# Optimization experiments

Hardware: AMD Instinct MI355X
Metric: run time of the kernel (lower is better)

## Reference

```python
import jax, jax.numpy as jnp
import numpy as np

N, E, H, HEADS, L, B = 16000, 256000, 192, 4, 4, 8
C = H // HEADS
VN, VE, T = 32, 8, 1000


def _sin_emb(t, dim):
    half = dim // 2
    freqs = jnp.exp(-np.log(10000.0) * jnp.arange(half, dtype=jnp.float32) / half)
    ang = t.astype(jnp.float32)[:, None] * freqs[None, :]
    return jnp.concatenate([jnp.sin(ang), jnp.cos(ang)], axis=-1)


def _ln(x, g, b, eps=1e-5):
    mu = jnp.mean(x, -1, keepdims=True)
    var = jnp.mean(jnp.square(x - mu), -1, keepdims=True)
    return (x - mu) * jax.lax.rsqrt(var + eps) * g + b


def setup_inputs():
    key = jax.random.key(0)
    ks = iter(jax.random.split(key, 64))
    p = lambda shape, s=0.02: jax.random.normal(next(ks), shape, jnp.float32) * s
    inp = {}
    inp['node_emb'] = p((VN, H))
    inp['edge_emb'] = p((VE, H))
    inp['time_w1'] = p((H, H)); inp['time_b1'] = jnp.zeros((H,), jnp.float32)
    inp['time_w2'] = p((H, H)); inp['time_b2'] = jnp.zeros((H,), jnp.float32)
    inp['mask_emb'] = p((2, H))
    inp['wq'] = p((L, H, H)); inp['bq'] = jnp.zeros((L, H), jnp.float32)
    inp['wk'] = p((L, H, H)); inp['bk'] = jnp.zeros((L, H), jnp.float32)
    inp['wv'] = p((L, H, H)); inp['bv'] = jnp.zeros((L, H), jnp.float32)
    inp['we'] = p((L, H, H))
    inp['wskip'] = p((L, H, H)); inp['bskip'] = jnp.zeros((L, H), jnp.float32)
    inp['wbeta'] = p((L, 3 * H))
    inp['ln_g'] = jnp.ones((L, H), jnp.float32); inp['ln_b'] = jnp.zeros((L, H), jnp.float32)
    inp['node_out_w'] = p((H, VN)); inp['node_out_b'] = jnp.zeros((VN,), jnp.float32)
    inp['edge_w1'] = p((4 * H, H)); inp['edge_b1'] = jnp.zeros((H,), jnp.float32)
    inp['edge_w2'] = p((H, VE)); inp['edge_b2'] = jnp.zeros((VE,), jnp.float32)
    inp['node_type'] = jax.random.randint(next(ks), (N,), 0, VN)
    inp['edge_type'] = jax.random.randint(next(ks), (E,), 0, VE)
    inp['edge_index'] = jax.random.randint(next(ks), (2, E), 0, N)
    inp['edit_mask'] = jax.random.randint(next(ks), (N,), 0, 2, dtype=jnp.int32)
    inp['node_batch'] = jnp.sort(jax.random.randint(next(ks), (N,), 0, B))
    inp['t_graph'] = jax.random.randint(next(ks), (B,), 1, T)
    return inp


def reference(node_emb, edge_emb, time_w1, time_b1, time_w2, time_b2, mask_emb,
              wq, bq, wk, bk, wv, bv, we, wskip, bskip, wbeta, ln_g, ln_b,
              node_out_w, node_out_b, edge_w1, edge_b1, edge_w2, edge_b2,
              node_type, edge_type, edge_index, edit_mask, node_batch, t_graph):
    src, dst = edge_index[0], edge_index[1]
    # time embedding: sinusoidal -> Linear -> SiLU -> Linear  => [B, H]
    t_vec = jax.nn.silu(_sin_emb(t_graph, H) @ time_w1 + time_b1) @ time_w2 + time_b2
    t_node = t_vec[node_batch]              # [N, H]
    t_edge = t_vec[node_batch[src]]         # [E, H]
    x = node_emb[node_type] + t_node + mask_emb[edit_mask]
    edge_attr = edge_emb[edge_type] + t_edge
    scale = 1.0 / np.sqrt(C)
    for l in range(L):
        q = (x @ wq[l] + bq[l]).reshape(N, HEADS, C)
        k = (x @ wk[l] + bk[l]).reshape(N, HEADS, C)
        v = (x @ wv[l] + bv[l]).reshape(N, HEADS, C)
        e = (edge_attr @ we[l]).reshape(E, HEADS, C)
        kj = k[src] + e                                   # [E, heads, C]
        score = jnp.sum(q[dst] * kj, axis=-1) * scale      # [E, heads]
        m = jax.ops.segment_max(score, dst, num_segments=N)
        ex = jnp.exp(score - m[dst])
        denom = jax.ops.segment_sum(ex, dst, num_segments=N)
        alpha = ex / denom[dst]
        msg = (v[src] + e) * alpha[..., None]              # [E, heads, C]
        out = jax.ops.segment_sum(msg, dst, num_segments=N).reshape(N, H)
        xr = x @ wskip[l] + bskip[l]
        beta = jax.nn.sigmoid(jnp.concatenate([out, xr, out - xr], -1) @ wbeta[l])[:, None]
        h = beta * xr + (1.0 - beta) * out
        x = _ln(x + h, ln_g[l], ln_b[l])
    node_logits = x @ node_out_w + node_out_b
    edge_feat = jnp.concatenate([x[src], x[dst], edge_attr, t_edge], -1)  # [E, 4H]
    edge_logits = jax.nn.silu(edge_feat @ edge_w1 + edge_b1) @ edge_w2 + edge_b2
    return node_logits, edge_logits
```

## Files before the change

### kernel.cpp

```cpp
#include <hip/hip_runtime.h>
#include <hip/hip_bf16.h>
#include <math.h>

#define NN 16000
#define NPAD 16128
#define NE 256000
#define H 192
#define RP 256
#define KVR 512
#define NL 4
#define NBATCH 8
#define VEt 8
#define HH (H*H)
#define EML 16

typedef __hip_bfloat16 bf16;
typedef unsigned short u16;
typedef unsigned char u8;
typedef unsigned int u32;
typedef __attribute__((ext_vector_type(8))) short bfrag_t;
typedef __attribute__((ext_vector_type(4))) float facc_t;
typedef __attribute__((ext_vector_type(4))) float f4;
typedef __attribute__((ext_vector_type(2))) unsigned int u32x2;

__device__ __forceinline__ bf16 f2b(float v){ return __float2bfloat16(v); }
__device__ __forceinline__ int rfl(int v){ return __builtin_amdgcn_readfirstlane(v); }

__device__ __forceinline__ unsigned enc8sw(float x){
    unsigned u = __float_as_uint(x);
    unsigned s = (u >> 24) & 0x80u;
    float ax = fabsf(x);
    if(ax >= 448.f) return s | 0x7Eu;
    if(ax < 0.015625f){
        int q = (int)rintf(ax * 512.f);
        return s | (unsigned)q;
    }
    unsigned au = u & 0x7FFFFFFFu;
    unsigned lsb = (au >> 20) & 1u;
    au += 0x7FFFFu + lsb;
    unsigned E = (au >> 23) - 127u;
    unsigned M = (au >> 20) & 7u;
    if((int)E > 8) return s | 0x7Eu;
    return s | ((E + 7u) << 3) | M;
}
__device__ __forceinline__ unsigned enc8(float x){
#if __has_builtin(__builtin_amdgcn_cvt_pk_fp8_f32)
    return (u32)__builtin_amdgcn_cvt_pk_fp8_f32(x, x, 0, false) & 0xFFu;
#else
    return enc8sw(x);
#endif
}
template<int SEL>
__device__ __forceinline__ float dec8s(u32 w){
#if __has_builtin(__builtin_amdgcn_cvt_f32_fp8)
    return __builtin_amdgcn_cvt_f32_fp8((int)w, SEL);
#else
    unsigned v = (w >> (SEL*8)) & 0xFFu;
    unsigned e = (v >> 3) & 15u, m = v & 7u;
    float mag = e ? __builtin_ldexpf((float)(8u + m), (int)e - 10)
                  : __builtin_ldexpf((float)m, -9);
    return (v & 0x80u) ? -mag : mag;
#endif
}
__device__ __forceinline__ float frcp(float x){
#if __has_builtin(__builtin_amdgcn_rcpf)
    return __builtin_amdgcn_rcpf(x);
#else
    return 1.f/x;
#endif
}

__global__ void k_sentinel(float* __restrict__ out, float v){ out[0] = v; }

__global__ void k_transpose(const float* __restrict__ wq, const float* __restrict__ wk,
                            const float* __restrict__ wv, const float* __restrict__ wsk,
                            const float* __restrict__ w1, const float* __restrict__ now,
                            const float* __restrict__ ew2, u16* __restrict__ wt){
    int mat = blockIdx.x;
    if(mat < 18){
        const float* src;
        if(mat < 4)       src = wq  + (size_t)mat*HH;
        else if(mat < 8)  src = wk  + (size_t)(mat-4)*HH;
        else if(mat < 12) src = wv  + (size_t)(mat-8)*HH;
        else if(mat < 16) src = wsk + (size_t)(mat-12)*HH;
        else              src = w1  + (size_t)(mat-16)*HH;
        u16* dst = wt + (size_t)mat*HH;
        const int slice = HH/8;
        int base = blockIdx.y*slice;
        for(int i = base + threadIdx.x; i < base + slice; i += blockDim.x){
            int k = i / H, n = i % H;
            bf16 b = f2b(src[i]);
            dst[n*H + k] = *(u16*)&b;
        }
    } else if(mat == 18){
        u16* dst = wt + (size_t)18*HH;
        const int slice = (32*192)/8;
        int base = blockIdx.y*slice;
        for(int i = base + threadIdx.x; i < base + slice; i += blockDim.x){
            int k = i >> 5, n = i & 31;
            bf16 b = f2b(now[i]);
            dst[n*192 + k] = *(u16*)&b;
        }
    } else {
        u16* dst = wt + (size_t)18*HH + 32*192;
        const int slice = (16*192)/8;
        int base = blockIdx.y*slice;
        for(int i = base + threadIdx.x; i < base + slice; i += blockDim.x){
            int k = i >> 4, n = i & 15;
            float v = (n < 8) ? ew2[k*8 + n] : 0.f;
            bf16 b = f2b(v);
            dst[n*192 + k] = *(u16*)&b;
        }
    }
}

__global__ void k_tvec(const int* __restrict__ tg, const float* __restrict__ w1,
                       const float* __restrict__ b1, const float* __restrict__ w2,
                       const float* __restrict__ b2, float* __restrict__ tvec){
    int b = blockIdx.x, j = threadIdx.x;
    __shared__ float emb[H], h1[H];
    float t = (float)tg[b];
    if(j < 96){
        float fr = __expf(-logf(10000.0f) * (float)j / 96.0f);
        float ang = t * fr;
        emb[j]      = sinf(ang);
        emb[j + 96] = cosf(ang);
    }
    __syncthreads();
    float acc = b1[j];
    for(int k = 0; k < H; k++) acc += emb[k] * w1[k*H + j];
    h1[j] = acc / (1.f + __expf(-acc));
    __syncthreads();
    float acc2 = b2[j];
    for(int k = 0; k < H; k++) acc2 += h1[k] * w2[k*H + j];
    tvec[b*H + j] = acc2;
}

__global__ void k_init_x(const float* __restrict__ nemb, const float* __restrict__ memb,
                         const float* __restrict__ tvec, const int* __restrict__ ntype,
                         const int* __restrict__ emask, const int* __restrict__ nbatch,
                         float* __restrict__ x, u16* __restrict__ xb){
    int idx = blockIdx.x*blockDim.x + threadIdx.x;
    if(idx >= NN*H) return;
    int n = idx / H, c = idx % H;
    float v = nemb[(size_t)ntype[n]*H + c] + tvec[nbatch[n]*H + c]
            + memb[(size_t)emask[n]*H + c];
    x[idx] = v;
    bf16 b = f2b(v); xb[idx] = *(u16*)&b;
}

__global__ void k_zero_i(int* __restrict__ p, int n){
    int i = blockIdx.x*blockDim.x + threadIdx.x;
    if(i < n) p[i] = 0;
}
__global__ void k_count(const int* __restrict__ edst, int* __restrict__ cnt){
    int e = blockIdx.x*blockDim.x + threadIdx.x;
    if(e < NE) atomicAdd(&cnt[edst[e]], 1);
}
__global__ __launch_bounds__(1024) void k_scan(const int* __restrict__ cnt,
                                               int* __restrict__ ofs, int* __restrict__ cur){
    __shared__ int wsum[16];
    __shared__ int carry_s;
    int tid = threadIdx.x, lane = tid & 63, w = tid >> 6;
    if(tid == 0) carry_s = 0;
    __syncthreads();
    for(int base = 0; base < NN; base += 1024){
        int idx = base + tid;
        int v = (idx < NN) ? cnt[idx] : 0;
        int sc = v;
        #pragma unroll
        for(int o = 1; o < 64; o <<= 1){
            int t = __shfl_up(sc, o);
            if(lane >= o) sc += t;
        }
        if(lane == 63) wsum[w] = sc;
        __syncthreads();
        if(w == 0){
            int ws = (lane < 16) ? wsum[lane] : 0;
            #pragma unroll
            for(int o = 1; o < 16; o <<= 1){
                int t = __shfl_up(ws, o);
                if(lane >= o) ws += t;
            }
            if(lane < 16) wsum[lane] = ws;
        }
        __syncthreads();
        int wbase = (w > 0) ? wsum[w-1] : 0;
        int c = carry_s;
        int excl = c + wbase + sc - v;
        if(idx < NN){ ofs[idx] = excl; cur[idx] = excl; }
        __syncthreads();
        if(tid == 0) carry_s = c + wsum[15];
        __syncthreads();
    }
    if(threadIdx.x == 0) ofs[NN] = carry_s;
}
__global__ void k_scatter(const int* __restrict__ esrc, const int* __restrict__ edst,
                          const int* __restrict__ etype, const int* __restrict__ nbatch,
                          int* __restrict__ cur, int2* __restrict__ spair){
    int e = blockIdx.x*blockDim.x + threadIdx.x;
    if(e >= NE) return;
    int s = esrc[e], d = edst[e];
    int pos = atomicAdd(&cur[d], 1);
    int2 se; se.x = s*KVR; se.y = (nbatch[s]*VEt + etype[e])*KVR;
    spair[pos] = se;
}

__global__ void k_etab(const float* __restrict__ eemb, const float* __restrict__ tvec,
                       const float* __restrict__ we, u16* __restrict__ etab){
    int blk = blockIdx.x;
    int l = blk >> 6, idx = blk & 63, b = idx >> 3, et = idx & 7;
    int c = threadIdx.x;
    __shared__ float a[H];
    a[c] = eemb[et*H + c] + tvec[b*H + c];
    __syncthreads();
    float acc = 0.f;
    const float* w = we + (size_t)l*HH;
    for(int k = 0; k < H; k++) acc += a[k] * w[k*H + c];
    bf16 bv = f2b(acc);
    etab[(size_t)blk*256 + (c/3)*4 + (c%3)] = *(u16*)&bv;
}

__global__ void k_ctab(const float* __restrict__ eemb, const float* __restrict__ tvec,
                       const float* __restrict__ w1, const float* __restrict__ b1,
                       u16* __restrict__ ctab){
    int idx = blockIdx.x, b = idx >> 3, et = idx & 7;
    int c = threadIdx.x;
    __shared__ float a[H];
    a[c] = eemb[et*H + c] + tvec[b*H + c];
    __syncthreads();
    float acc = b1[c];
    for(int k = 0; k < H; k++){
        acc += a[k]          * w1[(size_t)(2*H + k)*H + c];
        acc += tvec[b*H + k] * w1[(size_t)(3*H + k)*H + c];
    }
    bf16 bv = f2b(acc);
    ctab[(size_t)idx*256 + (c/3)*4 + (c%3)] = *(u16*)&bv;
}

struct GemmP {
    const u16* wt[4];
    const float* bias[4];
    void* out[4];
    int obf[4];
};
__global__ __launch_bounds__(256) void k_gemm(const u16* __restrict__ A, GemmP P){
    int oi = blockIdx.y / 3, nt = blockIdx.y % 3;
    const u16* Wt = P.wt[oi];
    const float* bias = P.bias[oi];
    int wave = rfl(threadIdx.x >> 6), lane = threadIdx.x & 63;
    int quad = lane >> 4, l16 = lane & 15;
    int m0 = blockIdx.x*256 + wave*64;
    int n0 = nt*64;
    facc_t acc[4][4];
    #pragma unroll
    for(int i = 0; i < 4; i++)
        #pragma unroll
        for(int j = 0; j < 4; j++){ acc[i][j][0]=0.f; acc[i][j][1]=0.f; acc[i][j][2]=0.f; acc[i][j][3]=0.f; }
    #pragma unroll
    for(int kc = 0; kc < 6; kc++){
        int kb = kc*32 + quad*8;
        bfrag_t af[4], bg[4];
        #pragma unroll
        for(int i = 0; i < 4; i++) af[i] = *(const bfrag_t*)(A  + (size_t)(m0 + i*16 + l16)*H + kb);
        #pragma unroll
        for(int j = 0; j < 4; j++) bg[j] = *(const bfrag_t*)(Wt + (size_t)(n0 + j*16 + l16)*H + kb);
        #pragma unroll
        for(int i = 0; i < 4; i++)
            #pragma unroll
            for(int j = 0; j < 4; j++)
                acc[i][j] = __builtin_amdgcn_mfma_f32_16x16x32_bf16(af[i], bg[j], acc[i][j], 0, 0, 0);
    }
    float bv[4];
    #pragma unroll
    for(int j = 0; j < 4; j++) bv[j] = bias ? bias[n0 + j*16 + l16] : 0.f;
    int mode = P.obf[oi];
    if(mode != 0){
        u8* out = (u8*)P.out[oi];
        int rstride = (mode == 2) ? RP : KVR;
        int mult    = (mode == 2) ? 4  : 8;
        int koff    = (mode == 4) ? 4  : 0;
        int byteoff[4];
        #pragma unroll
        for(int j = 0; j < 4; j++){
            int c = n0 + j*16 + l16;
            byteoff[j] = (c/3)*mult + (c%3) + koff;
        }
        #pragma unroll
        for(int i = 0; i < 4; i++){
            int rb = m0 + i*16 + quad*4;
            #pragma unroll
            for(int r = 0; r < 4; r++){
                int row = rb + r;
                if(row < NN){
                    #pragma unroll
                    for(int j = 0; j < 4; j++)
                        out[(size_t)row*rstride + byteoff[j]] = (u8)enc8(acc[i][j][r] + bv[j]);
                }
            }
        }
    } else {
        float* out = (float*)P.out[oi];
        #pragma unroll
        for(int i = 0; i < 4; i++){
            int rb = m0 + i*16 + quad*4;
            #pragma unroll
            for(int r = 0; r < 4; r++){
                int row = rb + r;
                if(row < NN){
                    #pragma unroll
                    for(int j = 0; j < 4; j++)
                        out[(size_t)row*H + n0 + j*16 + l16] = acc[i][j][r] + bv[j];
                }
            }
        }
    }
}

__global__ __launch_bounds__(256) void k_attn(
    const float* __restrict__ Q, const u8* __restrict__ KVb,
    const float* __restrict__ XR,
    const u16* __restrict__ etab, const int* __restrict__ ofs,
    const int2* __restrict__ spair,
    const float* __restrict__ wb, const float* __restrict__ lng, const float* __restrict__ lnb,
    float* __restrict__ x, u16* __restrict__ xb)
{
    int wv = rfl(threadIdx.x >> 6);
    int n = blockIdx.x*4 + wv;
    int lane = threadIdx.x & 63;
    int lane8 = lane*8;
    int ch = lane*3;
    size_t base = (size_t)n*H + ch;
    const float scale = 0.14433756729740646f;
    float q0 = Q[base], q1 = Q[base+1], q2 = Q[base+2];
    int p0 = ofs[n], p1 = ofs[n+1];
    float lac[4]  = {0.f,0.f,0.f,0.f};
    float ac0[4]  = {0.f,0.f,0.f,0.f};
    float ac1[4]  = {0.f,0.f,0.f,0.f};
    float ac2[4]  = {0.f,0.f,0.f,0.f};
    const u8* etb = (const u8*)etab;
    int p = p0;
    for(; p + 3 < p1; p += 4){
        int so[4], eo[4];
        #pragma unroll
        for(int t = 0; t < 4; t++){ so[t] = spair[p+t].x; eo[t] = spair[p+t].y; }
        u32x2 kv[4], ew[4];
        #pragma unroll
        for(int t = 0; t < 4; t++){
            kv[t] = *(const u32x2*)(KVb + so[t] + lane8);
            ew[t] = *(const u32x2*)(etb + eo[t] + lane8);
        }
        float e0[4], e1[4], e2[4], tt[4];
        #pragma unroll
        for(int t = 0; t < 4; t++){
            e0[t] = __uint_as_float(ew[t].x << 16);
            e1[t] = __uint_as_float(ew[t].x & 0xffff0000u);
            e2[t] = __uint_as_float(ew[t].y << 16);
            tt[t] = q0*(dec8s<0>(kv[t].x)+e0[t]) + q1*(dec8s<1>(kv[t].x)+e1[t])
                  + q2*(dec8s<2>(kv[t].x)+e2[t]);
        }
        #pragma unroll
        for(int o = 1; o <= 8; o <<= 1){
            #pragma unroll
            for(int t = 0; t < 4; t++) tt[t] += __shfl_xor(tt[t], o);
        }
        #pragma unroll
        for(int t = 0; t < 4; t++){
            float sc = fminf(fmaxf(tt[t]*scale, -60.f), 60.f);
            float pw = __expf(sc);
            lac[t] += pw;
            ac0[t] += pw*(dec8s<0>(kv[t].y)+e0[t]);
            ac1[t] += pw*(dec8s<1>(kv[t].y)+e1[t]);
            ac2[t] += pw*(dec8s<2>(kv[t].y)+e2[t]);
        }
    }
    for(; p < p1; p++){
        int soA = spair[p].x, eoA = spair[p].y;
        u32x2 kvA = *(const u32x2*)(KVb + soA + lane8);
        u32x2 ewA = *(const u32x2*)(etb + eoA + lane8);
        float e0A = __uint_as_float(ewA.x << 16);
        float e1A = __uint_as_float(ewA.x & 0xffff0000u);
        float e2A = __uint_as_float(ewA.y << 16);
        float tA = q0*(dec8s<0>(kvA.x)+e0A) + q1*(dec8s<1>(kvA.x)+e1A) + q2*(dec8s<2>(kvA.x)+e2A);
        tA += __shfl_xor(tA,1); tA += __shfl_xor(tA,2); tA += __shfl_xor(tA,4); tA += __shfl_xor(tA,8);
        float sc = fminf(fmaxf(tA*scale, -60.f), 60.f);
        float pw = __expf(sc);
        lac[0] += pw;
        ac0[0] += pw*(dec8s<0>(kvA.y)+e0A);
        ac1[0] += pw*(dec8s<1>(kvA.y)+e1A);
        ac2[0] += pw*(dec8s<2>(kvA.y)+e2A);
    }
    float l  = (lac[0]+lac[1]) + (lac[2]+lac[3]);
    float a0 = (ac0[0]+ac0[1]) + (ac0[2]+ac0[3]);
    float a1 = (ac1[0]+ac1[1]) + (ac1[2]+ac1[3]);
    float a2 = (ac2[0]+ac2[1]) + (ac2[2]+ac2[3]);
    float inv = (p1 > p0) ? 1.f/l : 0.f;
    float o0 = a0*inv, o1 = a1*inv, o2 = a2*inv;
    float xr0 = XR[base], xr1 = XR[base+1], xr2 = XR[base+2];
    float sd = o0*wb[ch]  + o1*wb[ch+1]  + o2*wb[ch+2]
             + xr0*wb[H+ch] + xr1*wb[H+ch+1] + xr2*wb[H+ch+2]
             + (o0-xr0)*wb[2*H+ch] + (o1-xr1)*wb[2*H+ch+1] + (o2-xr2)*wb[2*H+ch+2];
    sd += __shfl_xor(sd,1); sd += __shfl_xor(sd,2); sd += __shfl_xor(sd,4);
    sd += __shfl_xor(sd,8); sd += __shfl_xor(sd,16); sd += __shfl_xor(sd,32);
    float beta = 1.f/(1.f + __expf(-sd));
    float h0 = beta*xr0 + (1.f-beta)*o0;
    float h1 = beta*xr1 + (1.f-beta)*o1;
    float h2 = beta*xr2 + (1.f-beta)*o2;
    float y0 = x[base] + h0, y1 = x[base+1] + h1, y2 = x[base+2] + h2;
    float s3 = y0 + y1 + y2;
    float q3 = y0*y0 + y1*y1 + y2*y2;
    #pragma unroll
    for(int o = 1; o <= 32; o <<= 1){
        s3 += __shfl_xor(s3, o);
        q3 += __shfl_xor(q3, o);
    }
    float mean = s3 * (1.f/H);
    float var = fmaxf(q3*(1.f/H) - mean*mean, 0.f);
    float rs = rsqrtf(var + 1e-5f);
    float d0 = y0-mean, d1 = y1-mean, d2 = y2-mean;
    float z0 = d0*rs*lng[ch]   + lnb[ch];
    float z1 = d1*rs*lng[ch+1] + lnb[ch+1];
    float z2 = d2*rs*lng[ch+2] + lnb[ch+2];
    x[base] = z0; x[base+1] = z1; x[base+2] = z2;
    bf16 t0 = f2b(z0), t1 = f2b(z1), t2 = f2b(z2);
    xb[base] = *(u16*)&t0; xb[base+1] = *(u16*)&t1; xb[base+2] = *(u16*)&t2;
}

__global__ __launch_bounds__(256) void k_nodeout(const u16* __restrict__ A, const u16* __restrict__ Wt,
                                                 const float* __restrict__ b, float* __restrict__ out){
    int wave = rfl(threadIdx.x >> 6), lane = threadIdx.x & 63;
    int quad = lane >> 4, l16 = lane & 15;
    int m0 = blockIdx.x*256 + wave*64;
    facc_t acc[4][2];
    #pragma unroll
    for(int i = 0; i < 4; i++)
        #pragma unroll
        for(int j = 0; j < 2; j++){ acc[i][j][0]=0.f; acc[i][j][1]=0.f; acc[i][j][2]=0.f; acc[i][j][3]=0.f; }
    #pragma unroll
    for(int kc = 0; kc < 6; kc++){
        int kb = kc*32 + quad*8;
        bfrag_t af[4], bg[2];
        #pragma unroll
        for(int i = 0; i < 4; i++) af[i] = *(const bfrag_t*)(A  + (size_t)(m0 + i*16 + l16)*H + kb);
        #pragma unroll
        for(int j = 0; j < 2; j++) bg[j] = *(const bfrag_t*)(Wt + (size_t)(j*16 + l16)*H + kb);
        #pragma unroll
        for(int i = 0; i < 4; i++)
            #pragma unroll
            for(int j = 0; j < 2; j++)
                acc[i][j] = __builtin_amdgcn_mfma_f32_16x16x32_bf16(af[i], bg[j], acc[i][j], 0, 0, 0);
    }
    float bv[2];
    #pragma unroll
    for(int j = 0; j < 2; j++) bv[j] = b[j*16 + l16];
    #pragma unroll
    for(int i = 0; i < 4; i++){
        int rb = m0 + i*16 + quad*4;
        #pragma unroll
        for(int r = 0; r < 4; r++){
            int row = rb + r;
            if(row < NN){
                #pragma unroll
                for(int j = 0; j < 2; j++)
                    out[(size_t)row*32 + j*16 + l16] = acc[i][j][r] + bv[j];
            }
        }
    }
}

__global__ __launch_bounds__(256) void k_edgemlp(
    const int* __restrict__ esrc, const int* __restrict__ edst, const int* __restrict__ etype,
    const int* __restrict__ nb,
    const u8* __restrict__ xs1, const u8* __restrict__ xd1, const u16* __restrict__ ctab,
    const u16* __restrict__ w2t, const float* __restrict__ b2p, float* __restrict__ out)
{
    __shared__ u16 hbuf[4][16][200];
    int wave = rfl(threadIdx.x >> 6);
    int lane = threadIdx.x & 63;
    int lane8 = lane*8;
    int l16 = lane & 15, quad = lane >> 4;
    int wid = blockIdx.x*4 + wave;
    int e0 = wid*EML;
    const u8* ctb = (const u8*)ctab;
    bfrag_t bg[6];
    #pragma unroll
    for(int kc = 0; kc < 6; kc++)
        bg[kc] = *(const bfrag_t*)(w2t + (size_t)l16*192 + kc*32 + quad*8);
    for(int eb = 0; eb < EML; eb += 2){
        int eX = e0 + eb, eY = e0 + eb + 1;
        int sX = esrc[eX], dX = edst[eX];
        int sY = esrc[eY], dY = edst[eY];
        int coX = (nb[sX]*VEt + etype[eX])*KVR;
        int coY = (nb[sY]*VEt + etype[eY])*KVR;
        u32 awX = *(const u32*)(xs1 + (size_t)sX*RP + lane*4);
        u32 awY = *(const u32*)(xs1 + (size_t)sY*RP + lane*4);
        u32 bwX = *(const u32*)(xd1 + (size_t)dX*RP + lane*4);
        u32 bwY = *(const u32*)(xd1 + (size_t)dY*RP + lane*4);
        u32x2 cwX = *(const u32x2*)(ctb + coX + lane8);
        u32x2 cwY = *(const u32x2*)(ctb + coY + lane8);
        float cfX0 = __uint_as_float(cwX.x << 16);
        float cfX1 = __uint_as_float(cwX.x & 0xffff0000u);
        float cfX2 = __uint_as_float(cwX.y << 16);
        float cfY0 = __uint_as_float(cwY.x << 16);
        float cfY1 = __uint_as_float(cwY.x & 0xffff0000u);
        float cfY2 = __uint_as_float(cwY.y << 16);
        float hX0, hX1, hX2, hY0, hY1, hY2;
        { float v = dec8s<0>(awX)+dec8s<0>(bwX)+cfX0; hX0 = v*frcp(1.f+__expf(-v)); }
        { float v = dec8s<1>(awX)+dec8s<1>(bwX)+cfX1; hX1 = v*frcp(1.f+__expf(-v)); }
        { float v = dec8s<2>(awX)+dec8s<2>(bwX)+cfX2; hX2 = v*frcp(1.f+__expf(-v)); }
        { float v = dec8s<0>(awY)+dec8s<0>(bwY)+cfY0; hY0 = v*frcp(1.f+__expf(-v)); }
        { float v = dec8s<1>(awY)+dec8s<1>(bwY)+cfY1; hY1 = v*frcp(1.f+__expf(-v)); }
        { float v = dec8s<2>(awY)+dec8s<2>(bwY)+cfY2; hY2 = v*frcp(1.f+__expf(-v)); }
        u16* rowX = &hbuf[wave][eb][0];
        u16* rowY = &hbuf[wave][eb+1][0];
        bf16 x0 = f2b(hX0), x1 = f2b(hX1), x2 = f2b(hX2);
        bf16 y0 = f2b(hY0), y1 = f2b(hY1), y2 = f2b(hY2);
        rowX[lane*3+0] = *(u16*)&x0; rowX[lane*3+1] = *(u16*)&x1; rowX[lane*3+2] = *(u16*)&x2;
        rowY[lane*3+0] = *(u16*)&y0; rowY[lane*3+1] = *(u16*)&y1; rowY[lane*3+2] = *(u16*)&y2;
    }
    __syncthreads();
    facc_t acc;
    acc[0]=0.f; acc[1]=0.f; acc[2]=0.f; acc[3]=0.f;
    #pragma unroll
    for(int kc = 0; kc < 6; kc++){
        bfrag_t af = *(const bfrag_t*)&hbuf[wave][l16][kc*32 + quad*8];
        acc = __builtin_amdgcn_mfma_f32_16x16x32_bf16(af, bg[kc], acc, 0, 0, 0);
    }
    if(l16 < 8){
        float bo = b2p[l16];
        #pragma unroll
        for(int r = 0; r < 4; r++){
            int e = e0 + quad*4 + r;
            out[(size_t)e*8 + l16] = acc[r] + bo;
        }
    }
}

extern "C" void kernel_launch(void* const* d_in, const int* in_sizes, int n_in,
                              void* d_out, int out_size, void* d_ws, size_t ws_size,
                              hipStream_t stream)
{
    {
        int bad = -1;
        if(n_in != 31) bad = 100;
        else {
            const int chk_idx[9] = {0, 7, 16, 21, 23, 26, 27, 29, 30};
            const int chk_sz [9] = {32*H, NL*HH, NL*3*H, 4*HH, H*8, NE, 2*NE, NN, NBATCH};
            for(int i = 0; i < 9; i++) if(in_sizes[chk_idx[i]] != chk_sz[i]){ bad = chk_idx[i]; break; }
        }
        if(bad >= 0){ k_sentinel<<<1,1,0,stream>>>((float*)d_out, 20000.f + 256.f*bad); return; }
        if(out_size != NN*32 + NE*8){ k_sentinel<<<1,1,0,stream>>>((float*)d_out, 30000.f); return; }
    }

    const float* node_emb = (const float*)d_in[0];
    const float* edge_emb = (const float*)d_in[1];
    const float* time_w1  = (const float*)d_in[2];
    const float* time_b1  = (const float*)d_in[3];
    const float* time_w2  = (const float*)d_in[4];
    const float* time_b2  = (const float*)d_in[5];
    const float* mask_emb = (const float*)d_in[6];
    const float* wq       = (const float*)d_in[7];
    const float* bq       = (const float*)d_in[8];
    const float* wk       = (const float*)d_in[9];
    const float* bk       = (const float*)d_in[10];
    const float* wv       = (const float*)d_in[11];
    const float* bv       = (const float*)d_in[12];
    const float* we       = (const float*)d_in[13];
    const float* wskip    = (const float*)d_in[14];
    const float* bskip    = (const float*)d_in[15];
    const float* wbeta    = (const float*)d_in[16];
    const float* ln_g     = (const float*)d_in[17];
    const float* ln_b     = (const float*)d_in[18];
    const float* now      = (const float*)d_in[19];
    const float* nob      = (const float*)d_in[20];
    const float* ew1      = (const float*)d_in[21];
    const float* eb1      = (const float*)d_in[22];
    const float* ew2      = (const float*)d_in[23];
    const float* eb2      = (const float*)d_in[24];
    const int* node_type  = (const int*)d_in[25];
    const int* edge_type  = (const int*)d_in[26];
    const int* edge_index = (const int*)d_in[27];
    const int* edit_mask  = (const int*)d_in[28];
    const int* node_batch = (const int*)d_in[29];
    const int* t_graph    = (const int*)d_in[30];
    const int* esrc = edge_index;
    const int* edst = edge_index + NE;

    char* wsb = (char*)d_ws;
    size_t off = 0;
    auto take = [&](size_t bytes) -> char* {
        char* r = wsb + off;
        off += (bytes + 255) & ~(size_t)255;
        return r;
    };
    float* tvec = (float*)take((size_t)NBATCH*H*4);
    float* x    = (float*)take((size_t)NN*H*4);
    u16*   xb   = (u16*)  take((size_t)NPAD*H*2);
    float* Q    = (float*)take((size_t)NN*H*4);
    u8*    KVb  = (u8*)   take((size_t)NN*KVR);
    float* XR   = (float*)take((size_t)NN*H*4);
    u8*    xs1  = (u8*)   take((size_t)NN*RP);
    u8*    xd1  = (u8*)   take((size_t)NN*RP);
    u16*   etab = (u16*)  take((size_t)NL*64*KVR);
    u16*   ctab = (u16*)  take((size_t)64*KVR);
    u16*   wt   = (u16*)  take((size_t)(18*HH + 32*192 + 16*192)*2);
    int* cnt    = (int*)  take((size_t)(NN+1)*4);
    int* offa   = (int*)  take((size_t)(NN+1)*4);
    int* cur    = (int*)  take((size_t)(NN+1)*4);
    int2* spair = (int2*) take((size_t)NE*8);

    if(ws_size < off){
        k_sentinel<<<1,1,0,stream>>>((float*)d_out, 10000.f + (float)(ws_size >> 20));
        return;
    }

    u16* w32t = wt + (size_t)18*HH;
    u16* w2t  = w32t + 32*192;

    k_transpose<<<dim3(20, 8), 256, 0, stream>>>(wq, wk, wv, wskip, ew1, now, ew2, wt);
    k_tvec<<<NBATCH, H, 0, stream>>>(t_graph, time_w1, time_b1, time_w2, time_b2, tvec);
    k_init_x<<<(NN*H + 255)/256, 256, 0, stream>>>(node_emb, mask_emb, tvec, node_type,
                                                   edit_mask, node_batch, x, xb);
    k_zero_i<<<(NN + 255)/256, 256, 0, stream>>>(cnt, NN);
    k_count<<<NE/256, 256, 0, stream>>>(edst, cnt);
    k_scan<<<1, 1024, 0, stream>>>(cnt, offa, cur);
    k_scatter<<<NE/256, 256, 0, stream>>>(esrc, edst, edge_type, node_batch, cur, spair);
    k_etab<<<NL*64, H, 0, stream>>>(edge_emb, tvec, we, etab);
    k_ctab<<<64, H, 0, stream>>>(edge_emb, tvec, ew1, eb1, ctab);

    for(int l = 0; l < NL; l++){
        GemmP P;
        P.wt[0] = wt + (size_t)(0  + l)*HH;  P.bias[0] = bq   + (size_t)l*H;  P.out[0] = Q;   P.obf[0] = 0;
        P.wt[1] = wt + (size_t)(4  + l)*HH;  P.bias[1] = bk   + (size_t)l*H;  P.out[1] = KVb; P.obf[1] = 3;
        P.wt[2] = wt + (size_t)(8  + l)*HH;  P.bias[2] = bv   + (size_t)l*H;  P.out[2] = KVb; P.obf[2] = 4;
        P.wt[3] = wt + (size_t)(12 + l)*HH;  P.bias[3] = bskip+ (size_t)l*H;  P.out[3] = XR;  P.obf[3] = 0;
        k_gemm<<<dim3(63, 12), 256, 0, stream>>>(xb, P);
        k_attn<<<NN/4, 256, 0, stream>>>(Q, KVb, XR, etab + (size_t)l*64*256, offa, spair,
                                         wbeta + (size_t)l*3*H, ln_g + (size_t)l*H,
                                         ln_b + (size_t)l*H, x, xb);
    }
    {
        GemmP P;
        P.wt[0] = wt + (size_t)16*HH; P.bias[0] = nullptr; P.out[0] = xs1; P.obf[0] = 2;
        P.wt[1] = wt + (size_t)17*HH; P.bias[1] = nullptr; P.out[1] = xd1; P.obf[1] = 2;
        P.wt[2] = P.wt[0]; P.bias[2] = nullptr; P.out[2] = xs1; P.obf[2] = 2;
        P.wt[3] = P.wt[0]; P.bias[3] = nullptr; P.out[3] = xs1; P.obf[3] = 2;
        k_gemm<<<dim3(63, 6), 256, 0, stream>>>(xb, P);
    }
    k_nodeout<<<63, 256, 0, stream>>>(xb, w32t, nob, (float*)d_out);
    k_edgemlp<<<NE/(4*EML), 256, 0, stream>>>(esrc, edst, edge_type, node_batch, xs1, xd1, ctab,
                                              w2t, eb2, (float*)d_out + (size_t)NN*32);
}
```

Measured before the change: 504.3 us.

## Software-pipeline attention edge gathers and merge edge/coupling table kernels

The attention kernel's 4-edge loop now prefetches the next group's K/V and edge-embedding gathers into registers while computing the current group, so gather latency overlaps with arithmetic. Separately, the etab and ctab precompute kernels are merged into one launch to save a kernel launch. The double buffering raises register pressure, which may reduce occupancy in the attention kernel.

```diff
diff --git a/kernel.cpp b/kernel.cpp
--- a/kernel.cpp
+++ b/kernel.cpp
@@ -206,36 +206,34 @@
     spair[pos] = se;
 }
 
-__global__ void k_etab(const float* __restrict__ eemb, const float* __restrict__ tvec,
-                       const float* __restrict__ we, u16* __restrict__ etab){
+__global__ void k_tabs(const float* __restrict__ eemb, const float* __restrict__ tvec,
+                       const float* __restrict__ we,
+                       const float* __restrict__ w1, const float* __restrict__ b1,
+                       u16* __restrict__ etab, u16* __restrict__ ctab){
     int blk = blockIdx.x;
-    int l = blk >> 6, idx = blk & 63, b = idx >> 3, et = idx & 7;
     int c = threadIdx.x;
     __shared__ float a[H];
-    a[c] = eemb[et*H + c] + tvec[b*H + c];
-    __syncthreads();
-    float acc = 0.f;
-    const float* w = we + (size_t)l*HH;
-    for(int k = 0; k < H; k++) acc += a[k] * w[k*H + c];
-    bf16 bv = f2b(acc);
-    etab[(size_t)blk*256 + (c/3)*4 + (c%3)] = *(u16*)&bv;
-}
-
-__global__ void k_ctab(const float* __restrict__ eemb, const float* __restrict__ tvec,
-                       const float* __restrict__ w1, const float* __restrict__ b1,
-                       u16* __restrict__ ctab){
-    int idx = blockIdx.x, b = idx >> 3, et = idx & 7;
-    int c = threadIdx.x;
-    __shared__ float a[H];
-    a[c] = eemb[et*H + c] + tvec[b*H + c];
-    __syncthreads();
-    float acc = b1[c];
-    for(int k = 0; k < H; k++){
-        acc += a[k]          * w1[(size_t)(2*H + k)*H + c];
-        acc += tvec[b*H + k] * w1[(size_t)(3*H + k)*H + c];
-    }
-    bf16 bv = f2b(acc);
-    ctab[(size_t)idx*256 + (c/3)*4 + (c%3)] = *(u16*)&bv;
+    if(blk < NL*64){
+        int l = blk >> 6, idx = blk & 63, b = idx >> 3, et = idx & 7;
+        a[c] = eemb[et*H + c] + tvec[b*H + c];
+        __syncthreads();
+        float acc = 0.f;
+        const float* w = we + (size_t)l*HH;
+        for(int k = 0; k < H; k++) acc += a[k] * w[k*H + c];
+        bf16 bv = f2b(acc);
+        etab[(size_t)blk*256 + (c/3)*4 + (c%3)] = *(u16*)&bv;
+    } else {
+        int idx = blk - NL*64, b = idx >> 3, et = idx & 7;
+        a[c] = eemb[et*H + c] + tvec[b*H + c];
+        __syncthreads();
+        float acc = b1[c];
+        for(int k = 0; k < H; k++){
+            acc += a[k]          * w1[(size_t)(2*H + k)*H + c];
+            acc += tvec[b*H + k] * w1[(size_t)(3*H + k)*H + c];
+        }
+        bf16 bv = f2b(acc);
+        ctab[(size_t)idx*256 + (c/3)*4 + (c%3)] = *(u16*)&bv;
+    }
 }
 
 struct GemmP {
@@ -340,24 +338,36 @@
     float ac2[4]  = {0.f,0.f,0.f,0.f};
     const u8* etb = (const u8*)etab;
     int p = p0;
-    for(; p + 3 < p1; p += 4){
-        int so[4], eo[4];
-        #pragma unroll
-        for(int t = 0; t < 4; t++){ so[t] = spair[p+t].x; eo[t] = spair[p+t].y; }
-        u32x2 kv[4], ew[4];
+    u32x2 kvc[4], ewc[4];
+    bool have = (p + 3 < p1);
+    if(have){
         #pragma unroll
         for(int t = 0; t < 4; t++){
-            kv[t] = *(const u32x2*)(KVb + so[t] + lane8);
-            ew[t] = *(const u32x2*)(etb + eo[t] + lane8);
+            int2 se = spair[p+t];
+            kvc[t] = *(const u32x2*)(KVb + se.x + lane8);
+            ewc[t] = *(const u32x2*)(etb + se.y + lane8);
+        }
+    }
+    while(have){
+        int pn = p + 4;
+        bool more = (pn + 3 < p1);
+        u32x2 kvn[4], ewn[4];
+        if(more){
+            #pragma unroll
+            for(int t = 0; t < 4; t++){
+                int2 se = spair[pn+t];
+                kvn[t] = *(const u32x2*)(KVb + se.x + lane8);
+                ewn[t] = *(const u32x2*)(etb + se.y + lane8);
+            }
         }
         float e0[4], e1[4], e2[4], tt[4];
         #pragma unroll
         for(int t = 0; t < 4; t++){
-            e0[t] = __uint_as_float(ew[t].x << 16);
-            e1[t] = __uint_as_float(ew[t].x & 0xffff0000u);
-            e2[t] = __uint_as_float(ew[t].y << 16);
-            tt[t] = q0*(dec8s<0>(kv[t].x)+e0[t]) + q1*(dec8s<1>(kv[t].x)+e1[t])
-                  + q2*(dec8s<2>(kv[t].x)+e2[t]);
+            e0[t] = __uint_as_float(ewc[t].x << 16);
+            e1[t] = __uint_as_float(ewc[t].x & 0xffff0000u);
+            e2[t] = __uint_as_float(ewc[t].y << 16);
+            tt[t] = q0*(dec8s<0>(kvc[t].x)+e0[t]) + q1*(dec8s<1>(kvc[t].x)+e1[t])
+                  + q2*(dec8s<2>(kvc[t].x)+e2[t]);
         }
         #pragma unroll
         for(int o = 1; o <= 8; o <<= 1){
@@ -369,10 +379,16 @@
             float sc = fminf(fmaxf(tt[t]*scale, -60.f), 60.f);
             float pw = __expf(sc);
             lac[t] += pw;
-            ac0[t] += pw*(dec8s<0>(kv[t].y)+e0[t]);
-            ac1[t] += pw*(dec8s<1>(kv[t].y)+e1[t]);
-            ac2[t] += pw*(dec8s<2>(kv[t].y)+e2[t]);
-        }
+            ac0[t] += pw*(dec8s<0>(kvc[t].y)+e0[t]);
+            ac1[t] += pw*(dec8s<1>(kvc[t].y)+e1[t]);
+            ac2[t] += pw*(dec8s<2>(kvc[t].y)+e2[t]);
+        }
+        if(more){
+            #pragma unroll
+            for(int t = 0; t < 4; t++){ kvc[t] = kvn[t]; ewc[t] = ewn[t]; }
+        }
+        p = pn;
+        have = more;
     }
     for(; p < p1; p++){
         int soA = spair[p].x, eoA = spair[p].y;
@@ -625,8 +641,7 @@
     k_count<<<NE/256, 256, 0, stream>>>(edst, cnt);
     k_scan<<<1, 1024, 0, stream>>>(cnt, offa, cur);
     k_scatter<<<NE/256, 256, 0, stream>>>(esrc, edst, edge_type, node_batch, cur, spair);
-    k_etab<<<NL*64, H, 0, stream>>>(edge_emb, tvec, we, etab);
-    k_ctab<<<64, H, 0, stream>>>(edge_emb, tvec, ew1, eb1, ctab);
+    k_tabs<<<NL*64 + 64, H, 0, stream>>>(edge_emb, tvec, we, ew1, eb1, etab, ctab);
 
     for(int l = 0; l < NL; l++){
         GemmP P;
```

New measurement: 502.3 us. About the same (-0.4%).
